# Optimization experiments

Measured on AMD Instinct MI355X. Metric: run time of the kernel, lower is better.

Reference implementation:

```python
import jax, jax.numpy as jnp
import numpy as np

BLOCK = 32
EPS = 1e-8


def _box_avg(x, kernel):
    # x: [B,C,H,W]. Circular pad by BLOCK//2 on each side, then VALID depthwise
    # conv with a BLOCKxBLOCK averaging kernel -> output [B,C,H+1,W+1]
    # (matches torch Conv2d(kernel=32, padding=16, padding_mode='circular')).
    p = BLOCK // 2
    xp = jnp.pad(x, ((0, 0), (0, 0), (p, p), (p, p)), mode='wrap')
    C = x.shape[1]
    return jax.lax.conv_general_dilated(
        xp, kernel, window_strides=(1, 1), padding='VALID',
        feature_group_count=C,
        dimension_numbers=('NCHW', 'OIHW', 'NCHW'))


def setup_inputs() -> dict:
    key = jax.random.key(0)
    k1, k2 = jax.random.split(key)
    B, C, H, W = 16, 5, 512, 512
    img1 = jax.random.uniform(k1, (B, C, H, W), dtype=jnp.float32)
    img2 = jax.random.uniform(k2, (B, C, H, W), dtype=jnp.float32)
    # frozen depthwise box-filter weights: [C,1,BLOCK,BLOCK] = 1/BLOCK^2
    kernel = jnp.ones((C, 1, BLOCK, BLOCK), jnp.float32) / (BLOCK * BLOCK)
    return {"img1": img1, "img2": img2, "kernel": kernel}


def reference(img1, img2, kernel):
    mu1 = _box_avg(img1, kernel)
    mu2 = _box_avg(img2, kernel)
    mu1_sq = mu1 * mu1
    mu2_sq = mu2 * mu2
    mu1_mu2 = mu1 * mu2
    # Faithful to the source: it calls avg_conv(img1) (NOT img1**2) here,
    # so sigma*_sq = mu* - mu*_sq exactly as the original computes.
    sigma1_sq = mu1 - mu1_sq
    sigma2_sq = mu2 - mu2_sq
    sigma12 = _box_avg(img1 * img2, kernel) - mu1_mu2

    s = sigma1_sq + sigma2_sq
    m = mu1_sq + mu2_sq
    s_safe = jnp.where(s > EPS, s, 1.0)  # only used where s > EPS
    m_safe = jnp.where(m > EPS, m, 1.0)  # only used where m > EPS

    q = jnp.ones_like(s)  # default where no mask matches
    q = jnp.where((s < EPS) & (m > EPS), 2.0 * mu1_mu2 / m_safe, q)
    q = jnp.where((s > EPS) & (m < EPS), 2.0 * sigma12 / s_safe, q)
    q = jnp.where((s > EPS) & (m > EPS),
                  4.0 * mu1_mu2 * sigma12 / (m_safe * s_safe), q)
    return jnp.mean(q)
```

## Files before the change

### kernel.cpp

```cpp
#include <hip/hip_runtime.h>


#define HH 512
#define WW 512
#define NPLANES 80
#define BH 16
#define BANDS (HH/BH)
#define NBLOCKS (NPLANES*BANDS)
#define EPSF 1e-8f
#define INV_K (1.0f/1024.0f)

__device__ __forceinline__ void load8(const float* __restrict__ p, float a[8]) {
    const float4* v = reinterpret_cast<const float4*>(p);
    float4 x = v[0], y = v[1];
    a[0]=x.x; a[1]=x.y; a[2]=x.z; a[3]=x.w;
    a[4]=y.x; a[5]=y.y; a[6]=y.z; a[7]=y.w;
}

__device__ __forceinline__ void hwin(const float V[8], int lane, float Wo[8]) {
    float pz[8];
    pz[0] = V[0];
#pragma unroll
    for (int k = 1; k < 8; ++k) pz[k] = pz[k-1] + V[k];
    float t = pz[7];
    float u    = t + __shfl(t, (lane+1)&63);
    float base = u + __shfl(u, (lane+62)&63);
    float pm2[7], pp2[7];
#pragma unroll
    for (int k = 0; k < 7; ++k) pm2[k] = __shfl(pz[k], (lane+62)&63);
#pragma unroll
    for (int k = 0; k < 7; ++k) pp2[k] = __shfl(pz[k], (lane+ 2)&63);
    Wo[0] = base;
#pragma unroll
    for (int k = 1; k < 8; ++k) Wo[k] = base - pm2[k-1] + pp2[k-1];
}

__global__ __launch_bounds__(64)
void uiqi_main(const float* __restrict__ img1, const float* __restrict__ img2,
               double* __restrict__ partial)
{
    const int lane = threadIdx.x;
    const int bid  = blockIdx.x;

    const int xcd   = bid & 7;
    const int slot  = bid >> 3;
    const int band  = slot & 31;
    const int plane = xcd + 8*(slot >> 5);
    const int row0  = band*BH;
    const int j0    = lane*8;

    const float* p1 = img1 + (size_t)plane*HH*WW;
    const float* p2 = img2 + (size_t)plane*HH*WW;

    float V1[8], V2[8], V12[8];
#pragma unroll
    for (int k = 0; k < 8; ++k) { V1[k]=0.f; V2[k]=0.f; V12[k]=0.f; }

#pragma unroll 4
    for (int r = row0-16; r < row0+16; ++r) {
        int rm = r & (HH-1);
        float a[8], b[8];
        load8(p1 + rm*WW + j0, a);
        load8(p2 + rm*WW + j0, b);
#pragma unroll
        for (int k = 0; k < 8; ++k) {
            V1[k]  += a[k];
            V2[k]  += b[k];
            V12[k] += a[k]*b[k];
        }
    }

    double acc = 0.0;
    float na[8], nb[8], nc[8], nd[8];

    for (int i = row0; i < row0 + BH; ++i) {
        const bool more = (i != row0 + BH - 1);
        if (more) {
            int radd = (i+16) & (HH-1);
            int rsub = (i-16) & (HH-1);
            load8(p1 + radd*WW + j0, na);
            load8(p2 + radd*WW + j0, nb);
            load8(p1 + rsub*WW + j0, nc);
            load8(p2 + rsub*WW + j0, nd);
        }

        float W1[8], W2[8], W12[8];
        hwin(V1,  lane, W1);
        hwin(V2,  lane, W2);
        hwin(V12, lane, W12);

        float rowsum = 0.f;
        float q0save = 0.f;
#pragma unroll
        for (int k = 0; k < 8; ++k) {
            float mu1  = W1[k]*INV_K, mu2 = W2[k]*INV_K, mu12 = W12[k]*INV_K;
            float m11  = mu1*mu1, m22 = mu2*mu2, m12 = mu1*mu2;
            float s    = (mu1 - m11) + (mu2 - m22);
            float m    = m11 + m22;
            float sig  = mu12 - m12;
            bool  sg = s > EPSF, mg = m > EPSF, sl = s < EPSF, ml = m < EPSF;
            float num = 1.0f, den = 1.0f;
            if (sl && mg) { num = 2.0f*m12;     den = m;   }
            if (sg && ml) { num = 2.0f*sig;     den = s;   }
            if (sg && mg) { num = 4.0f*m12*sig; den = m*s; }
            float q = num * __builtin_amdgcn_rcpf(den);
            rowsum += q;
            if (k == 0) q0save = q;
        }
        if (lane == 0) rowsum += q0save;
        float wrow = (i == 0) ? 2.0f : 1.0f;
        acc += (double)rowsum * (double)wrow;

        if (more) {
#pragma unroll
            for (int k = 0; k < 8; ++k) {
                V1[k]  += na[k] - nc[k];
                V2[k]  += nb[k] - nd[k];
                V12[k] += na[k]*nb[k] - nc[k]*nd[k];
            }
        }
    }

#pragma unroll
    for (int s = 32; s > 0; s >>= 1) acc += __shfl_down(acc, s);
    if (lane == 0) partial[bid] = acc;
}

__global__ __launch_bounds__(256)
void uiqi_finalize(const double* __restrict__ partial, float* __restrict__ out)
{
    __shared__ double sred[256];
    double a = 0.0;
    for (int i = threadIdx.x; i < NBLOCKS; i += 256) a += partial[i];
    sred[threadIdx.x] = a;
    __syncthreads();
    for (int s = 128; s > 0; s >>= 1) {
        if (threadIdx.x < s) sred[threadIdx.x] += sred[threadIdx.x+s];
        __syncthreads();
    }
    if (threadIdx.x == 0) out[0] = (float)(sred[0] / 21053520.0);
}

extern "C" void kernel_launch(void* const* d_in, const int* in_sizes, int n_in,
                              void* d_out, int out_size, void* d_ws, size_t ws_size,
                              hipStream_t stream)
{
    const float* img1 = (const float*)d_in[0];
    const float* img2 = (const float*)d_in[1];
    double* partial = (double*)d_ws;
    uiqi_main<<<NBLOCKS, 64, 0, stream>>>(img1, img2, partial);
    uiqi_finalize<<<1, 256, 0, stream>>>(partial, (float*)d_out);
}
```

Baseline: 230.6 us.

## Halve band height and pack four wavefronts per block

Each wave now handles an 8-row band instead of 16, and four waves are grouped into a 256-thread block covering adjacent bands of the same plane. This raises wave count and occupancy so more memory latency is hidden. The cost is more redundant 32-row vertical warm-up reads per output row. The per-row accumulation is also switched from double to float, with a fully unrolled row loop, which loses some precision in the partial sums.

```diff
diff --git a/kernel.cpp b/kernel.cpp
--- a/kernel.cpp
+++ b/kernel.cpp
@@ -4,9 +4,12 @@
 #define HH 512
 #define WW 512
 #define NPLANES 80
-#define BH 16
+#define BH 8
+#define WPB 4
 #define BANDS (HH/BH)
-#define NBLOCKS (NPLANES*BANDS)
+#define BLOCKS_PER_PLANE (BANDS/WPB)
+#define NBLOCKS (NPLANES*BLOCKS_PER_PLANE)
+#define NPART (NBLOCKS*WPB)
 #define EPSF 1e-8f
 #define INV_K (1.0f/1024.0f)
 
@@ -35,19 +38,22 @@
     for (int k = 1; k < 8; ++k) Wo[k] = base - pm2[k-1] + pp2[k-1];
 }
 
-__global__ __launch_bounds__(64)
+__global__ __launch_bounds__(256, 8)
 void uiqi_main(const float* __restrict__ img1, const float* __restrict__ img2,
                double* __restrict__ partial)
 {
-    const int lane = threadIdx.x;
+    const int tid  = threadIdx.x;
+    const int lane = tid & 63;
+    const int wv   = tid >> 6;
     const int bid  = blockIdx.x;
 
-    const int xcd   = bid & 7;
-    const int slot  = bid >> 3;
-    const int band  = slot & 31;
-    const int plane = xcd + 8*(slot >> 5);
-    const int row0  = band*BH;
-    const int j0    = lane*8;
+    const int xcd    = bid & 7;
+    const int slot   = bid >> 3;
+    const int blkrow = slot & 15;
+    const int plane  = xcd + 8*(slot >> 4);
+    const int band   = blkrow*WPB + wv;
+    const int row0   = band*BH;
+    const int j0     = lane*8;
 
     const float* p1 = img1 + (size_t)plane*HH*WW;
     const float* p2 = img2 + (size_t)plane*HH*WW;
@@ -56,7 +62,7 @@
 #pragma unroll
     for (int k = 0; k < 8; ++k) { V1[k]=0.f; V2[k]=0.f; V12[k]=0.f; }
 
-#pragma unroll 4
+#pragma unroll 8
     for (int r = row0-16; r < row0+16; ++r) {
         int rm = r & (HH-1);
         float a[8], b[8];
@@ -70,11 +76,13 @@
         }
     }
 
-    double acc = 0.0;
-    float na[8], nb[8], nc[8], nd[8];
+    float accf = 0.f;
 
-    for (int i = row0; i < row0 + BH; ++i) {
-        const bool more = (i != row0 + BH - 1);
+#pragma unroll
+    for (int ii = 0; ii < BH; ++ii) {
+        const int i = row0 + ii;
+        const bool more = (ii != BH-1);
+        float na[8], nb[8], nc[8], nd[8];
         if (more) {
             int radd = (i+16) & (HH-1);
             int rsub = (i-16) & (HH-1);
@@ -108,8 +116,7 @@
             if (k == 0) q0save = q;
         }
         if (lane == 0) rowsum += q0save;
-        float wrow = (i == 0) ? 2.0f : 1.0f;
-        acc += (double)rowsum * (double)wrow;
+        accf += (i == 0) ? 2.0f*rowsum : rowsum;
 
         if (more) {
 #pragma unroll
@@ -121,9 +128,10 @@
         }
     }
 
+    double acc = (double)accf;
 #pragma unroll
     for (int s = 32; s > 0; s >>= 1) acc += __shfl_down(acc, s);
-    if (lane == 0) partial[bid] = acc;
+    if (lane == 0) partial[bid*WPB + wv] = acc;
 }
 
 __global__ __launch_bounds__(256)
@@ -131,7 +139,7 @@
 {
     __shared__ double sred[256];
     double a = 0.0;
-    for (int i = threadIdx.x; i < NBLOCKS; i += 256) a += partial[i];
+    for (int i = threadIdx.x; i < NPART; i += 256) a += partial[i];
     sred[threadIdx.x] = a;
     __syncthreads();
     for (int s = 128; s > 0; s >>= 1) {
@@ -148,6 +156,6 @@
     const float* img1 = (const float*)d_in[0];
     const float* img2 = (const float*)d_in[1];
     double* partial = (double*)d_ws;
-    uiqi_main<<<NBLOCKS, 64, 0, stream>>>(img1, img2, partial);
+    uiqi_main<<<NBLOCKS, 256, 0, stream>>>(img1, img2, partial);
     uiqi_finalize<<<1, 256, 0, stream>>>(partial, (float*)d_out);
 }
```

Result: slower. 484.4 us (+110.0%).
